# Optimization experiments

Hardware: AMD Instinct MI355X
Metric: run time of the kernel (lower is better)

The kernel has to match this reference:

```python
import jax, jax.numpy as jnp
import numpy as np

N = 100_000          # nodes
E = 3_200_000        # edges (avg degree 32)
EMB = 16             # item embedding dim
IN = EMB + 1         # concat(embed, scalar feature)
HID = 32             # GAT hidden size
NEMB = 1000          # embedding vocab
SLOPE = 0.2          # GATConv leaky_relu negative slope


def setup_inputs() -> dict:
    key = jax.random.key(0)
    ks = jax.random.split(key, 24)
    g = lambda k, shape, fan: jax.random.normal(k, shape, dtype=jnp.float32) * (1.0 / np.sqrt(fan))
    inp = {
        "x_ids": jax.random.randint(ks[0], (N,), 0, NEMB, dtype=jnp.int32),
        "x_feat": jax.random.normal(ks[1], (N, 1), dtype=jnp.float32),
        "src": jax.random.randint(ks[2], (E,), 0, N, dtype=jnp.int32),
        "dst": jax.random.randint(ks[3], (E,), 0, N, dtype=jnp.int32),
        "edge_attr": jax.random.normal(ks[4], (E, 1), dtype=jnp.float32),
        # embedding table
        "emb": g(ks[5], (NEMB, EMB), EMB),
        # GATConv 1 (in=17, out=32, heads=1, edge_dim=1)
        "W1": g(ks[6], (IN, HID), IN),
        "a_s1": g(ks[7], (HID,), HID),
        "a_d1": g(ks[8], (HID,), HID),
        "We1": g(ks[9], (1, HID), 1),
        "a_e1": g(ks[10], (HID,), HID),
        "b1": jnp.zeros((HID,), jnp.float32),
        # GATConv 2 (in=32, out=32)
        "W2": g(ks[11], (HID, HID), HID),
        "a_s2": g(ks[12], (HID,), HID),
        "a_d2": g(ks[13], (HID,), HID),
        "We2": g(ks[14], (1, HID), 1),
        "a_e2": g(ks[15], (HID,), HID),
        "b2": jnp.zeros((HID,), jnp.float32),
        # final linear (32 -> 1)
        "lin_w": g(ks[16], (HID, 1), HID),
        "lin_b": jnp.zeros((1,), jnp.float32),
    }
    return inp


def _gat_conv(x, src, dst, eattr, W, a_s, a_d, We, a_e, b):
    """PyG GATConv (heads=1, concat=True) with edge features, self-loops already added."""
    h = x @ W                                   # [N, HID]
    alpha_src = h @ a_s                         # [N]
    alpha_dst = h @ a_d                         # [N]
    alpha_edge = (eattr @ We) @ a_e             # [E']
    alpha = jax.nn.leaky_relu(alpha_src[src] + alpha_dst[dst] + alpha_edge, SLOPE)
    # segment softmax over incoming edges of each dst node
    m = jax.ops.segment_max(alpha, dst, num_segments=N)
    ex = jnp.exp(alpha - m[dst])
    denom = jax.ops.segment_sum(ex, dst, num_segments=N)
    coef = ex / (denom[dst] + 1e-16)
    out = jax.ops.segment_sum(coef[:, None] * h[src], dst, num_segments=N)
    return out + b


def reference(x_ids, x_feat, src, dst, edge_attr, emb,
              W1, a_s1, a_d1, We1, a_e1, b1,
              W2, a_s2, a_d2, We2, a_e2, b2,
              lin_w, lin_b):
    # embedding lookup + concat scalar feature -> [N, 17]
    x = jnp.concatenate([emb[x_ids], x_feat], axis=1)

    # add self-loops once; self-loop edge_attr = mean of incoming edge attrs (fill_value='mean')
    loop = jnp.arange(N, dtype=src.dtype)
    deg = jax.ops.segment_sum(jnp.ones((E,), x.dtype), dst, num_segments=N)
    loop_attr = jax.ops.segment_sum(edge_attr, dst, num_segments=N) / jnp.maximum(deg, 1.0)[:, None]
    src2 = jnp.concatenate([src, loop])
    dst2 = jnp.concatenate([dst, loop])
    ea2 = jnp.concatenate([edge_attr, loop_attr], axis=0)

    x = _gat_conv(x, src2, dst2, ea2, W1, a_s1, a_d1, We1, a_e1, b1)
    x = jax.nn.relu(x)  # dropout is identity in eval mode
    x = _gat_conv(x, src2, dst2, ea2, W2, a_s2, a_d2, We2, a_e2, b2)
    return x @ lin_w + lin_b  # [N, 1]
```

## Files before the change

kernel.cpp:

```cpp
#include <hip/hip_runtime.h>
#include <hip/hip_fp16.h>

#define NN 100000
#define EE 3200000
#define SLOPE 0.2f

#define BKN 128
constexpr int NBK = (NN + BKN - 1) / BKN;
#define CAP 4544
#define EPB 4096
constexpr int NBB = (EE + EPB - 1) / EPB;
constexpr int NBT = (NN + 255) / 256;
#define SUBN 1344
constexpr int NSB = NBK * 4;

__global__ void k_fat(const int* __restrict__ src, const int* __restrict__ dst,
                      const float* __restrict__ ea, int* __restrict__ cnt,
                      int2* __restrict__ stage,
                      const int* __restrict__ ids, const float* __restrict__ feat,
                      const float* __restrict__ emb, const float* __restrict__ W,
                      const float* __restrict__ avs, const float* __restrict__ avd,
                      __half* __restrict__ h, float* __restrict__ as_,
                      float* __restrict__ ad_) {
    __shared__ int hst[NBK];
    __shared__ int scl[NBK];
    __shared__ int gdel[NBK];
    __shared__ int aux[256];
    __shared__ int2 rec[EPB];
    __shared__ int addr[EPB];
    int t = threadIdx.x;
    if (blockIdx.x < NBB) {
        int base = blockIdx.x * EPB;
        int nedge = min(EPB, EE - base);
        for (int i = t; i < NBK; i += 256) hst[i] = 0;
        __syncthreads();
        int ds[16], ss[16]; float es[16];
#pragma unroll
        for (int j = 0; j < 16; j++) {
            int e = base + j * 256 + t;
            bool v = e < EE;
            ds[j] = v ? dst[e] : -1;
            ss[j] = v ? src[e] : 0;
            es[j] = v ? ea[e] : 0.f;
            if (v) atomicAdd(&hst[ds[j] >> 7], 1);
        }
        __syncthreads();
        int i0 = t * 4;
        int v0 = (i0 + 0 < NBK) ? hst[i0 + 0] : 0;
        int v1 = (i0 + 1 < NBK) ? hst[i0 + 1] : 0;
        int v2 = (i0 + 2 < NBK) ? hst[i0 + 2] : 0;
        int v3 = (i0 + 3 < NBK) ? hst[i0 + 3] : 0;
        int tsum = v0 + v1 + v2 + v3;
        aux[t] = tsum;
        __syncthreads();
        for (int off = 1; off < 256; off <<= 1) {
            int x = (t >= off) ? aux[t - off] : 0;
            __syncthreads();
            aux[t] += x;
            __syncthreads();
        }
        int ex = aux[t] - tsum;
        if (i0 + 0 < NBK) scl[i0 + 0] = ex;
        if (i0 + 1 < NBK) scl[i0 + 1] = ex + v0;
        if (i0 + 2 < NBK) scl[i0 + 2] = ex + v0 + v1;
        if (i0 + 3 < NBK) scl[i0 + 3] = ex + v0 + v1 + v2;
        __syncthreads();
        for (int i = t; i < NBK; i += 256) {
            int hh = hst[i];
            int g = hh ? atomicAdd(&cnt[i], hh) : 0;
            gdel[i] = (g + i * CAP) - scl[i];
        }
        __syncthreads();
#pragma unroll
        for (int j = 0; j < 16; j++) {
            if (ds[j] >= 0) {
                int bk = ds[j] >> 7;
                int pos = atomicAdd(&scl[bk], 1);
                int gpos = pos + gdel[bk];
                rec[pos] = make_int2(ss[j] | ((ds[j] & 127) << 17), __float_as_int(es[j]));
                addr[pos] = (gpos - bk * CAP < CAP) ? gpos : -1;
            }
        }
        __syncthreads();
        for (int i = t; i < nedge; i += 256) {
            int a = addr[i];
            if (a >= 0) stage[a] = rec[i];
        }
    } else {
        int n = (blockIdx.x - NBB) * 256 + t;
        if (n >= NN) return;
        float hv[32];
#pragma unroll
        for (int j = 0; j < 32; j++) hv[j] = 0.f;
        int id = ids[n];
        const float4* e4 = (const float4*)(emb + (size_t)id * 16);
#pragma unroll
        for (int k4 = 0; k4 < 4; k4++) {
            float4 xv = e4[k4];
            const float* wr = W + k4 * 4 * 32;
#pragma unroll
            for (int j = 0; j < 32; j++)
                hv[j] += xv.x * wr[j] + xv.y * wr[32 + j] + xv.z * wr[64 + j] + xv.w * wr[96 + j];
        }
        float f = feat[n];
#pragma unroll
        for (int j = 0; j < 32; j++) hv[j] += f * W[16 * 32 + j];
        float s = 0.f, d = 0.f;
#pragma unroll
        for (int j = 0; j < 32; j++) { s += hv[j] * avs[j]; d += hv[j] * avd[j]; }
        as_[n] = s;
        ad_[n] = d;
        __half2 tmp[16];
#pragma unroll
        for (int q = 0; q < 16; q++) tmp[q] = __floats2half2_rn(hv[2 * q], hv[2 * q + 1]);
        uint4* dst4 = (uint4*)(h + (size_t)n * 32);
        const uint4* s4 = (const uint4*)tmp;
#pragma unroll
        for (int q = 0; q < 4; q++) dst4[q] = s4[q];
    }
}

#define GATHER8(XB)                                                                   \
    for (int j = 0; j < m; j += 32) {                                                 \
        int2 p0 = XB[j + g];      int2 p1 = XB[j + 4 + g];                            \
        int2 p2 = XB[j + 8 + g];  int2 p3 = XB[j + 12 + g];                           \
        int2 p4 = XB[j + 16 + g]; int2 p5 = XB[j + 20 + g];                           \
        int2 p6 = XB[j + 24 + g]; int2 p7 = XB[j + 28 + g];                           \
        float2 h0 = __half22float2(*(const __half2*)(h + p0.x + cp));                 \
        float2 h1 = __half22float2(*(const __half2*)(h + p1.x + cp));                 \
        float2 h2 = __half22float2(*(const __half2*)(h + p2.x + cp));                 \
        float2 h3 = __half22float2(*(const __half2*)(h + p3.x + cp));                 \
        float2 h4 = __half22float2(*(const __half2*)(h + p4.x + cp));                 \
        float2 h5 = __half22float2(*(const __half2*)(h + p5.x + cp));                 \
        float2 h6 = __half22float2(*(const __half2*)(h + p6.x + cp));                 \
        float2 h7 = __half22float2(*(const __half2*)(h + p7.x + cp));                 \
        float w0 = __int_as_float(p0.y), w1 = __int_as_float(p1.y);                   \
        float w2 = __int_as_float(p2.y), w3 = __int_as_float(p3.y);                   \
        float w4 = __int_as_float(p4.y), w5 = __int_as_float(p5.y);                   \
        float w6 = __int_as_float(p6.y), w7 = __int_as_float(p7.y);                   \
        acc0.x += w0 * h0.x + w4 * h4.x; acc0.y += w0 * h0.y + w4 * h4.y;             \
        acc1.x += w1 * h1.x + w5 * h5.x; acc1.y += w1 * h1.y + w5 * h5.y;             \
        acc2.x += w2 * h2.x + w6 * h6.x; acc2.y += w2 * h2.y + w6 * h6.y;             \
        acc3.x += w3 * h3.x + w7 * h7.x; acc3.y += w3 * h3.y + w7 * h7.y;             \
    }

__global__ __launch_bounds__(256, 8) void k_l1(
    const int* __restrict__ cnt, const int2* __restrict__ stage,
    const __half* __restrict__ h, const float* __restrict__ as_,
    const float* __restrict__ ad_, const float* __restrict__ We,
    const float* __restrict__ ae, const float* __restrict__ bias,
    const float* __restrict__ W2, const float* __restrict__ avs2,
    const float* __restrict__ avd2, __half* __restrict__ hout,
    float* __restrict__ as2, float* __restrict__ ad2,
    int2* __restrict__ csr, int2* __restrict__ offs2) {
    __shared__ int2 ebuf[SUBN];
    __shared__ int2 xb[4][64];
    __shared__ float w2s[1024];
    __shared__ float xrow[4][32];
    __shared__ int ldeg[32];
    __shared__ float esum[32];
    __shared__ int starts[32];
    __shared__ int lcur[32];
    __shared__ int cnts[32];
    __shared__ float means[32];
    int t = threadIdx.x;
    int p = blockIdx.x;
    int b2 = (p & 7) * 391 + (p >> 3);
    int b = b2 >> 2, q = b2 & 3;
    int nbase = b * BKN + q * 32;
    int npb = min(32, NN - nbase);
    if (npb <= 0) return;
    int lane = t & 63;
    int wid = t >> 6;
    int g = lane >> 4;
    int cp = (lane & 15) * 2;
    int comp = lane & 31;
    float ce = We[comp] * ae[comp];
#pragma unroll
    for (int off = 1; off < 32; off <<= 1) ce += __shfl_xor(ce, off);

    if (t < 32) { ldeg[t] = 0; esum[t] = 0.f; }
    for (int i = t; i < 1024; i += 256) w2s[i] = W2[i];
    __syncthreads();
    int c = min(cnt[b], CAP);
    const int2* ep = stage + (size_t)b * CAP;
    for (int i = t; i < c; i += 256) {
        int2 e = ep[i];
        int dl = (e.x >> 17) & 127;
        if ((dl >> 5) == q) {
            atomicAdd(&ldeg[dl & 31], 1);
            atomicAdd(&esum[dl & 31], __int_as_float(e.y));
        }
    }
    __syncthreads();
    if (t < 64) {
        int l = lane;
        int dv = (l < npb) ? ldeg[l] + 1 : 0;
        int v = dv;
#pragma unroll
        for (int off = 1; off < 32; off <<= 1) {
            int x = __shfl_up(v, off);
            if (lane >= off) v += x;
        }
        if (l < 32) {
            int st = v - dv;
            starts[l] = st;
            lcur[l] = st;
            cnts[l] = dv;
            means[l] = esum[l] / fmaxf((float)ldeg[l], 1.0f);
        }
    }
    __syncthreads();
    for (int i = t; i < c; i += 256) {
        int2 e = ep[i];
        int dl = (e.x >> 17) & 127;
        if ((dl >> 5) == q) {
            int pos = atomicAdd(&lcur[dl & 31], 1);
            if (pos < SUBN) ebuf[pos] = make_int2(e.x & 0x1FFFF, e.y);
        }
    }
    __syncthreads();
    if (t < npb) {
        int pp = lcur[t];
        if (pp < SUBN) ebuf[pp] = make_int2(nbase + t, __float_as_int(means[t]));
    }
    __syncthreads();
    int tot = min(starts[31] + cnts[31], SUBN);
    int2* cw = csr + (size_t)b2 * SUBN;
    for (int i = t; i < tot; i += 256) cw[i] = ebuf[i];
    if (t < npb) {
        int st = starts[t];
        int cn = cnts[t];
        if (st >= SUBN) { st = 0; cn = 0; }
        else if (cn > SUBN - st) cn = SUBN - st;
        offs2[nbase + t] = make_int2(b2 * SUBN + st, cn);
    }

    for (int i2 = 0; i2 < 8; i2++) {
        int n = wid * 8 + i2;
        if (n >= npb) break;
        int gn = nbase + n;
        int base2 = starts[n];
        int cn = cnts[n];
        if (base2 >= SUBN) cn = 0;
        else if (cn > SUBN - base2) cn = SUBN - base2;
        float adn = ad_[gn];
        float2 acc0 = {0.f, 0.f}, acc1 = {0.f, 0.f}, acc2 = {0.f, 0.f}, acc3 = {0.f, 0.f};
        float exs = 0.f;
        for (int cb = 0; cb < cn; cb += 64) {
            int idx = cb + lane;
            bool val = idx < cn;
            int2 e = ebuf[base2 + (val ? idx : 0)];
            float a = as_[e.x] + adn + ce * __int_as_float(e.y);
            a = (a >= 0.f) ? a : SLOPE * a;
            float ex = val ? __expf(a) : 0.f;
            exs += ex;
            xb[wid][lane] = make_int2(e.x << 5, __float_as_int(ex));
            int m = min(cn - cb, 64);
            GATHER8(xb[wid])
        }
        float2 acc;
        acc.x = (acc0.x + acc1.x) + (acc2.x + acc3.x);
        acc.y = (acc0.y + acc1.y) + (acc2.y + acc3.y);
        acc.x += __shfl_xor(acc.x, 16); acc.y += __shfl_xor(acc.y, 16);
        acc.x += __shfl_xor(acc.x, 32); acc.y += __shfl_xor(acc.y, 32);
#pragma unroll
        for (int off = 1; off < 64; off <<= 1) exs += __shfl_xor(exs, off);
        float inv = 1.0f / (exs + 1e-16f);
        float ox = acc.x * inv + bias[cp];
        float oy = acc.y * inv + bias[cp + 1];
        ox = fmaxf(ox, 0.f);
        oy = fmaxf(oy, 0.f);
        if (lane < 16) { xrow[wid][cp] = ox; xrow[wid][cp + 1] = oy; }
        float hx = 0.f, hy = 0.f;
#pragma unroll
        for (int k = 0; k < 32; k++) {
            float xk = xrow[wid][k];
            hx += xk * w2s[k * 32 + cp];
            hy += xk * w2s[k * 32 + cp + 1];
        }
        float ps = hx * avs2[cp] + hy * avs2[cp + 1];
        float pd = hx * avd2[cp] + hy * avd2[cp + 1];
#pragma unroll
        for (int off = 1; off < 16; off <<= 1) {
            ps += __shfl_xor(ps, off);
            pd += __shfl_xor(pd, off);
        }
        if (lane == 0) { as2[gn] = ps; ad2[gn] = pd; }
        if (lane < 16)
            *(__half2*)(hout + ((size_t)gn << 5) + cp) = __floats2half2_rn(hx, hy);
    }
}

__global__ void k_gat(const int2* __restrict__ offs2, const int2* __restrict__ csr,
                      const __half* __restrict__ h, const float* __restrict__ as_,
                      const float* __restrict__ ad_,
                      const float* __restrict__ We, const float* __restrict__ ae,
                      const float* __restrict__ bias,
                      const float* __restrict__ lw, const float* __restrict__ lb,
                      float* __restrict__ out) {
    __shared__ int2 xb[4][64];
    int wid = threadIdx.x >> 6;
    int node = blockIdx.x * 4 + wid;
    int lane = threadIdx.x & 63;
    int comp = lane & 31;
    int cp = (lane & 15) * 2;
    int g = lane >> 4;
    float c = We[comp] * ae[comp];
#pragma unroll
    for (int off = 1; off < 32; off <<= 1) c += __shfl_xor(c, off);
    int2 oo = offs2[node];
    int base = oo.x;
    int cnt = oo.y;
    float adn = ad_[node];
    float2 acc0 = {0.f, 0.f}, acc1 = {0.f, 0.f}, acc2 = {0.f, 0.f}, acc3 = {0.f, 0.f};
    float exs = 0.f;
    for (int cb = 0; cb < cnt; cb += 64) {
        int idx = cb + lane;
        bool val = idx < cnt;
        int2 e = csr[base + (val ? idx : 0)];
        float a = as_[e.x] + adn + c * __int_as_float(e.y);
        a = (a >= 0.f) ? a : SLOPE * a;
        float ex = val ? __expf(a) : 0.f;
        exs += ex;
        xb[wid][lane] = make_int2(e.x << 5, __float_as_int(ex));
        int m = min(cnt - cb, 64);
        GATHER8(xb[wid])
    }
    float2 acc;
    acc.x = (acc0.x + acc1.x) + (acc2.x + acc3.x);
    acc.y = (acc0.y + acc1.y) + (acc2.y + acc3.y);
    acc.x += __shfl_xor(acc.x, 16); acc.y += __shfl_xor(acc.y, 16);
    acc.x += __shfl_xor(acc.x, 32); acc.y += __shfl_xor(acc.y, 32);
#pragma unroll
    for (int off = 1; off < 64; off <<= 1) exs += __shfl_xor(exs, off);
    float inv = 1.0f / (exs + 1e-16f);
    float ox = acc.x * inv + bias[cp];
    float oy = acc.y * inv + bias[cp + 1];
    float y = ox * lw[cp] + oy * lw[cp + 1];
#pragma unroll
    for (int off = 1; off < 16; off <<= 1) y += __shfl_xor(y, off);
    if (lane == 0) out[node] = y + lb[0];
}


extern "C" void kernel_launch(void* const* d_in, const int* in_sizes, int n_in,
                              void* d_out, int out_size, void* d_ws, size_t ws_size,
                              hipStream_t stream) {
    const int* x_ids = (const int*)d_in[0];
    const float* x_feat = (const float*)d_in[1];
    const int* src = (const int*)d_in[2];
    const int* dst = (const int*)d_in[3];
    const float* eattr = (const float*)d_in[4];
    const float* emb = (const float*)d_in[5];
    const float* W1 = (const float*)d_in[6];
    const float* a_s1 = (const float*)d_in[7];
    const float* a_d1 = (const float*)d_in[8];
    const float* We1 = (const float*)d_in[9];
    const float* a_e1 = (const float*)d_in[10];
    const float* b1 = (const float*)d_in[11];
    const float* W2 = (const float*)d_in[12];
    const float* a_s2 = (const float*)d_in[13];
    const float* a_d2 = (const float*)d_in[14];
    const float* We2 = (const float*)d_in[15];
    const float* a_e2 = (const float*)d_in[16];
    const float* b2 = (const float*)d_in[17];
    const float* lin_w = (const float*)d_in[18];
    const float* lin_b = (const float*)d_in[19];

    char* p = (char*)d_ws;
    auto alloc = [&](size_t bytes) {
        void* r = (void*)p;
        p += (bytes + 255) & ~(size_t)255;
        return r;
    };
    int* cnt = (int*)alloc(NBK * 4);
    int2* offs2 = (int2*)alloc((size_t)NN * 8);
    float* asb1 = (float*)alloc(NN * 4);
    float* adb1 = (float*)alloc(NN * 4);
    float* asb2 = (float*)alloc(NN * 4);
    float* adb2 = (float*)alloc(NN * 4);
    __half* h1 = (__half*)alloc((size_t)NN * 32 * 2);
    __half* h2 = (__half*)alloc((size_t)NN * 32 * 2);
    int2* csr = (int2*)alloc((size_t)NSB * SUBN * 8);
    int2* stage = (int2*)alloc((size_t)NBK * CAP * 8);
    (void)ws_size; (void)in_sizes; (void)n_in; (void)out_size;

    hipMemsetAsync(cnt, 0, NBK * 4, stream);

    k_fat<<<NBB + NBT, 256, 0, stream>>>(src, dst, eattr, cnt, stage,
                                         x_ids, x_feat, emb, W1, a_s1, a_d1,
                                         h1, asb1, adb1);
    k_l1<<<NSB, 256, 0, stream>>>(cnt, stage, h1, asb1, adb1,
                                  We1, a_e1, b1,
                                  W2, a_s2, a_d2, h2, asb2, adb2,
                                  csr, offs2);
    k_gat<<<(NN + 3) / 4, 256, 0, stream>>>(offs2, csr, h2, asb2, adb2,
                                            We2, a_e2, b2,
                                            lin_w, lin_b, (float*)d_out);
}
```

Baseline: 317.6 us.

## Bucket edges directly into 32-node global bins with atomics, drop block-local sort

Replaces the block-local histogram/scan/scatter partitioning with direct per-edge global atomicAdd into 3125 buckets of 32 destination nodes each, writing staged records straight to global memory. The layer-1 kernel now processes one 32-node bucket per block without filtering a 128-node bucket four times, loading edges into registers once. The gather macro is also narrowed from 8 to 4 edges per iteration. This trades coalesced staged writes and fewer atomics for many contended global atomics and scattered stores, and removes capacity clamps, so overflow safety now depends on CAPS/SUBN bounds and on the random degree distribution of the test inputs.

Measured after the change: 745.9 us. 2.35x slower.

```diff
diff --git a/kernel.cpp b/kernel.cpp
--- a/kernel.cpp
+++ b/kernel.cpp
@@ -5,14 +5,12 @@
 #define EE 3200000
 #define SLOPE 0.2f
 
-#define BKN 128
-constexpr int NBK = (NN + BKN - 1) / BKN;
-#define CAP 4544
-#define EPB 4096
-constexpr int NBB = (EE + EPB - 1) / EPB;
+#define CAPS 1344
+#define SUBN 1376
+constexpr int NSB2 = NN / 32;
+#define EPB2 2048
+constexpr int NAB = (EE + EPB2 - 1) / EPB2;
 constexpr int NBT = (NN + 255) / 256;
-#define SUBN 1344
-constexpr int NSB = NBK * 4;
 
 __global__ void k_fat(const int* __restrict__ src, const int* __restrict__ dst,
                       const float* __restrict__ ea, int* __restrict__ cnt,
@@ -22,72 +20,23 @@
                       const float* __restrict__ avs, const float* __restrict__ avd,
                       __half* __restrict__ h, float* __restrict__ as_,
                       float* __restrict__ ad_) {
-    __shared__ int hst[NBK];
-    __shared__ int scl[NBK];
-    __shared__ int gdel[NBK];
-    __shared__ int aux[256];
-    __shared__ int2 rec[EPB];
-    __shared__ int addr[EPB];
     int t = threadIdx.x;
-    if (blockIdx.x < NBB) {
-        int base = blockIdx.x * EPB;
-        int nedge = min(EPB, EE - base);
-        for (int i = t; i < NBK; i += 256) hst[i] = 0;
-        __syncthreads();
-        int ds[16], ss[16]; float es[16];
-#pragma unroll
-        for (int j = 0; j < 16; j++) {
+    if (blockIdx.x < NAB) {
+        int base = blockIdx.x * EPB2;
+#pragma unroll
+        for (int j = 0; j < 8; j++) {
             int e = base + j * 256 + t;
-            bool v = e < EE;
-            ds[j] = v ? dst[e] : -1;
-            ss[j] = v ? src[e] : 0;
-            es[j] = v ? ea[e] : 0.f;
-            if (v) atomicAdd(&hst[ds[j] >> 7], 1);
-        }
-        __syncthreads();
-        int i0 = t * 4;
-        int v0 = (i0 + 0 < NBK) ? hst[i0 + 0] : 0;
-        int v1 = (i0 + 1 < NBK) ? hst[i0 + 1] : 0;
-        int v2 = (i0 + 2 < NBK) ? hst[i0 + 2] : 0;
-        int v3 = (i0 + 3 < NBK) ? hst[i0 + 3] : 0;
-        int tsum = v0 + v1 + v2 + v3;
-        aux[t] = tsum;
-        __syncthreads();
-        for (int off = 1; off < 256; off <<= 1) {
-            int x = (t >= off) ? aux[t - off] : 0;
-            __syncthreads();
-            aux[t] += x;
-            __syncthreads();
-        }
-        int ex = aux[t] - tsum;
-        if (i0 + 0 < NBK) scl[i0 + 0] = ex;
-        if (i0 + 1 < NBK) scl[i0 + 1] = ex + v0;
-        if (i0 + 2 < NBK) scl[i0 + 2] = ex + v0 + v1;
-        if (i0 + 3 < NBK) scl[i0 + 3] = ex + v0 + v1 + v2;
-        __syncthreads();
-        for (int i = t; i < NBK; i += 256) {
-            int hh = hst[i];
-            int g = hh ? atomicAdd(&cnt[i], hh) : 0;
-            gdel[i] = (g + i * CAP) - scl[i];
-        }
-        __syncthreads();
-#pragma unroll
-        for (int j = 0; j < 16; j++) {
-            if (ds[j] >= 0) {
-                int bk = ds[j] >> 7;
-                int pos = atomicAdd(&scl[bk], 1);
-                int gpos = pos + gdel[bk];
-                rec[pos] = make_int2(ss[j] | ((ds[j] & 127) << 17), __float_as_int(es[j]));
-                addr[pos] = (gpos - bk * CAP < CAP) ? gpos : -1;
+            if (e < EE) {
+                int d = dst[e];
+                int bk = d >> 5;
+                int pos = atomicAdd(&cnt[bk], 1);
+                if (pos < CAPS)
+                    stage[(size_t)bk * CAPS + pos] =
+                        make_int2(src[e] | ((d & 31) << 17), __float_as_int(ea[e]));
             }
         }
-        __syncthreads();
-        for (int i = t; i < nedge; i += 256) {
-            int a = addr[i];
-            if (a >= 0) stage[a] = rec[i];
-        }
     } else {
-        int n = (blockIdx.x - NBB) * 256 + t;
+        int n = (blockIdx.x - NAB) * 256 + t;
         if (n >= NN) return;
         float hv[32];
 #pragma unroll
@@ -120,28 +69,22 @@
     }
 }
 
-#define GATHER8(XB)                                                                   \
-    for (int j = 0; j < m; j += 32) {                                                 \
-        int2 p0 = XB[j + g];      int2 p1 = XB[j + 4 + g];                            \
-        int2 p2 = XB[j + 8 + g];  int2 p3 = XB[j + 12 + g];                           \
-        int2 p4 = XB[j + 16 + g]; int2 p5 = XB[j + 20 + g];                           \
-        int2 p6 = XB[j + 24 + g]; int2 p7 = XB[j + 28 + g];                           \
+#define GATHER4(XB)                                                                   \
+    for (int j = 0; j < m; j += 16) {                                                 \
+        int2 p0 = XB[j + g];                                                          \
+        int2 p1 = XB[j + 4 + g];                                                      \
+        int2 p2 = XB[j + 8 + g];                                                      \
+        int2 p3 = XB[j + 12 + g];                                                     \
         float2 h0 = __half22float2(*(const __half2*)(h + p0.x + cp));                 \
         float2 h1 = __half22float2(*(const __half2*)(h + p1.x + cp));                 \
         float2 h2 = __half22float2(*(const __half2*)(h + p2.x + cp));                 \
         float2 h3 = __half22float2(*(const __half2*)(h + p3.x + cp));                 \
-        float2 h4 = __half22float2(*(const __half2*)(h + p4.x + cp));                 \
-        float2 h5 = __half22float2(*(const __half2*)(h + p5.x + cp));                 \
-        float2 h6 = __half22float2(*(const __half2*)(h + p6.x + cp));                 \
-        float2 h7 = __half22float2(*(const __half2*)(h + p7.x + cp));                 \
         float w0 = __int_as_float(p0.y), w1 = __int_as_float(p1.y);                   \
         float w2 = __int_as_float(p2.y), w3 = __int_as_float(p3.y);                   \
-        float w4 = __int_as_float(p4.y), w5 = __int_as_float(p5.y);                   \
-        float w6 = __int_as_float(p6.y), w7 = __int_as_float(p7.y);                   \
-        acc0.x += w0 * h0.x + w4 * h4.x; acc0.y += w0 * h0.y + w4 * h4.y;             \
-        acc1.x += w1 * h1.x + w5 * h5.x; acc1.y += w1 * h1.y + w5 * h5.y;             \
-        acc2.x += w2 * h2.x + w6 * h6.x; acc2.y += w2 * h2.y + w6 * h6.y;             \
-        acc3.x += w3 * h3.x + w7 * h7.x; acc3.y += w3 * h3.y + w7 * h7.y;             \
+        acc0.x += w0 * h0.x; acc0.y += w0 * h0.y;                                     \
+        acc1.x += w1 * h1.x; acc1.y += w1 * h1.y;                                     \
+        acc2.x += w2 * h2.x; acc2.y += w2 * h2.y;                                     \
+        acc3.x += w3 * h3.x; acc3.y += w3 * h3.y;                                     \
     }
 
 __global__ __launch_bounds__(256, 8) void k_l1(
@@ -164,12 +107,8 @@
     __shared__ int cnts[32];
     __shared__ float means[32];
     int t = threadIdx.x;
-    int p = blockIdx.x;
-    int b2 = (p & 7) * 391 + (p >> 3);
-    int b = b2 >> 2, q = b2 & 3;
-    int nbase = b * BKN + q * 32;
-    int npb = min(32, NN - nbase);
-    if (npb <= 0) return;
+    int bb = blockIdx.x;
+    int nbase = bb * 32;
     int lane = t & 63;
     int wid = t >> 6;
     int g = lane >> 4;
@@ -182,20 +121,26 @@
     if (t < 32) { ldeg[t] = 0; esum[t] = 0.f; }
     for (int i = t; i < 1024; i += 256) w2s[i] = W2[i];
     __syncthreads();
-    int c = min(cnt[b], CAP);
-    const int2* ep = stage + (size_t)b * CAP;
-    for (int i = t; i < c; i += 256) {
-        int2 e = ep[i];
-        int dl = (e.x >> 17) & 127;
-        if ((dl >> 5) == q) {
-            atomicAdd(&ldeg[dl & 31], 1);
-            atomicAdd(&esum[dl & 31], __int_as_float(e.y));
+    int c = min(cnt[bb], CAPS);
+    const int2* ep = stage + (size_t)bb * CAPS;
+    int2 er[6];
+#pragma unroll
+    for (int j = 0; j < 6; j++) {
+        int i = j * 256 + t;
+        er[j] = (i < c) ? ep[i] : make_int2(-1, 0);
+    }
+#pragma unroll
+    for (int j = 0; j < 6; j++) {
+        if (er[j].x >= 0) {
+            int dl = (er[j].x >> 17) & 31;
+            atomicAdd(&ldeg[dl], 1);
+            atomicAdd(&esum[dl], __int_as_float(er[j].y));
         }
     }
     __syncthreads();
     if (t < 64) {
         int l = lane;
-        int dv = (l < npb) ? ldeg[l] + 1 : 0;
+        int dv = (l < 32) ? ldeg[l] + 1 : 0;
         int v = dv;
 #pragma unroll
         for (int off = 1; off < 32; off <<= 1) {
@@ -211,39 +156,29 @@
         }
     }
     __syncthreads();
-    for (int i = t; i < c; i += 256) {
-        int2 e = ep[i];
-        int dl = (e.x >> 17) & 127;
-        if ((dl >> 5) == q) {
-            int pos = atomicAdd(&lcur[dl & 31], 1);
-            if (pos < SUBN) ebuf[pos] = make_int2(e.x & 0x1FFFF, e.y);
-        }
-    }
-    __syncthreads();
-    if (t < npb) {
-        int pp = lcur[t];
-        if (pp < SUBN) ebuf[pp] = make_int2(nbase + t, __float_as_int(means[t]));
-    }
-    __syncthreads();
-    int tot = min(starts[31] + cnts[31], SUBN);
-    int2* cw = csr + (size_t)b2 * SUBN;
+#pragma unroll
+    for (int j = 0; j < 6; j++) {
+        if (er[j].x >= 0) {
+            int dl = (er[j].x >> 17) & 31;
+            int pos = atomicAdd(&lcur[dl], 1);
+            ebuf[pos] = make_int2(er[j].x & 0x1FFFF, er[j].y);
+        }
+    }
+    __syncthreads();
+    if (t < 32)
+        ebuf[lcur[t]] = make_int2(nbase + t, __float_as_int(means[t]));
+    __syncthreads();
+    int tot = starts[31] + cnts[31];
+    int2* cw = csr + (size_t)bb * SUBN;
     for (int i = t; i < tot; i += 256) cw[i] = ebuf[i];
-    if (t < npb) {
-        int st = starts[t];
-        int cn = cnts[t];
-        if (st >= SUBN) { st = 0; cn = 0; }
-        else if (cn > SUBN - st) cn = SUBN - st;
-        offs2[nbase + t] = make_int2(b2 * SUBN + st, cn);
-    }
+    if (t < 32)
+        offs2[nbase + t] = make_int2(bb * SUBN + starts[t], cnts[t]);
 
     for (int i2 = 0; i2 < 8; i2++) {
         int n = wid * 8 + i2;
-        if (n >= npb) break;
         int gn = nbase + n;
         int base2 = starts[n];
         int cn = cnts[n];
-        if (base2 >= SUBN) cn = 0;
-        else if (cn > SUBN - base2) cn = SUBN - base2;
         float adn = ad_[gn];
         float2 acc0 = {0.f, 0.f}, acc1 = {0.f, 0.f}, acc2 = {0.f, 0.f}, acc3 = {0.f, 0.f};
         float exs = 0.f;
@@ -257,7 +192,7 @@
             exs += ex;
             xb[wid][lane] = make_int2(e.x << 5, __float_as_int(ex));
             int m = min(cn - cb, 64);
-            GATHER8(xb[wid])
+            GATHER4(xb[wid])
         }
         float2 acc;
         acc.x = (acc0.x + acc1.x) + (acc2.x + acc3.x);
@@ -325,7 +260,7 @@
         exs += ex;
         xb[wid][lane] = make_int2(e.x << 5, __float_as_int(ex));
         int m = min(cnt - cb, 64);
-        GATHER8(xb[wid])
+        GATHER4(xb[wid])
     }
     float2 acc;
     acc.x = (acc0.x + acc1.x) + (acc2.x + acc3.x);
@@ -374,7 +309,7 @@
         p += (bytes + 255) & ~(size_t)255;
         return r;
     };
-    int* cnt = (int*)alloc(NBK * 4);
+    int* cnt = (int*)alloc(NSB2 * 4);
     int2* offs2 = (int2*)alloc((size_t)NN * 8);
     float* asb1 = (float*)alloc(NN * 4);
     float* adb1 = (float*)alloc(NN * 4);
@@ -382,19 +317,19 @@
     float* adb2 = (float*)alloc(NN * 4);
     __half* h1 = (__half*)alloc((size_t)NN * 32 * 2);
     __half* h2 = (__half*)alloc((size_t)NN * 32 * 2);
-    int2* csr = (int2*)alloc((size_t)NSB * SUBN * 8);
-    int2* stage = (int2*)alloc((size_t)NBK * CAP * 8);
+    int2* csr = (int2*)alloc((size_t)NSB2 * SUBN * 8);
+    int2* stage = (int2*)alloc((size_t)NSB2 * CAPS * 8);
     (void)ws_size; (void)in_sizes; (void)n_in; (void)out_size;
 
-    hipMemsetAsync(cnt, 0, NBK * 4, stream);
-
-    k_fat<<<NBB + NBT, 256, 0, stream>>>(src, dst, eattr, cnt, stage,
+    hipMemsetAsync(cnt, 0, NSB2 * 4, stream);
+
+    k_fat<<<NAB + NBT, 256, 0, stream>>>(src, dst, eattr, cnt, stage,
                                          x_ids, x_feat, emb, W1, a_s1, a_d1,
                                          h1, asb1, adb1);
-    k_l1<<<NSB, 256, 0, stream>>>(cnt, stage, h1, asb1, adb1,
-                                  We1, a_e1, b1,
-                                  W2, a_s2, a_d2, h2, asb2, adb2,
-                                  csr, offs2);
+    k_l1<<<NSB2, 256, 0, stream>>>(cnt, stage, h1, asb1, adb1,
+                                   We1, a_e1, b1,
+                                   W2, a_s2, a_d2, h2, asb2, adb2,
+                                   csr, offs2);
     k_gat<<<(NN + 3) / 4, 256, 0, stream>>>(offs2, csr, h2, asb2, adb2,
                                             We2, a_e2, b2,
                                             lin_w, lin_b, (float*)d_out);
```

## Scatter edges directly to stage, use wave-shuffle scan, shrink gather unroll

Applied to the files above, without the earlier changes.

The binning kernel no longer stages per-block records and addresses in LDS. Each thread now writes its packed edge straight to the global stage buffer, which cuts about 48KB of shared memory per block and one sync pass, but the global writes are no longer coalesced. The block prefix scan now uses wave shuffles plus a 4-entry cross-wave sum instead of a barrier-heavy LDS scan. The gather macro is reduced from 8 to 4 loads per iteration, which avoids wasted work when a chunk holds fewer than 32 edges, at the cost of less memory-level parallelism.

Result: no change. 316.7 us (-0.3%).

```diff
diff --git a/kernel.cpp b/kernel.cpp
--- a/kernel.cpp
+++ b/kernel.cpp
@@ -25,13 +25,11 @@
     __shared__ int hst[NBK];
     __shared__ int scl[NBK];
     __shared__ int gdel[NBK];
-    __shared__ int aux[256];
-    __shared__ int2 rec[EPB];
-    __shared__ int addr[EPB];
+    __shared__ int wsum[4];
     int t = threadIdx.x;
     if (blockIdx.x < NBB) {
         int base = blockIdx.x * EPB;
-        int nedge = min(EPB, EE - base);
+        int lane = t & 63, wid = t >> 6;
         for (int i = t; i < NBK; i += 256) hst[i] = 0;
         __syncthreads();
         int ds[16], ss[16]; float es[16];
@@ -51,15 +49,18 @@
         int v2 = (i0 + 2 < NBK) ? hst[i0 + 2] : 0;
         int v3 = (i0 + 3 < NBK) ? hst[i0 + 3] : 0;
         int tsum = v0 + v1 + v2 + v3;
-        aux[t] = tsum;
-        __syncthreads();
-        for (int off = 1; off < 256; off <<= 1) {
-            int x = (t >= off) ? aux[t - off] : 0;
-            __syncthreads();
-            aux[t] += x;
-            __syncthreads();
-        }
-        int ex = aux[t] - tsum;
+        int incl = tsum;
+#pragma unroll
+        for (int off = 1; off < 64; off <<= 1) {
+            int x = __shfl_up(incl, off);
+            if (lane >= off) incl += x;
+        }
+        if (lane == 63) wsum[wid] = incl;
+        __syncthreads();
+        int wpre = 0;
+#pragma unroll
+        for (int w = 0; w < 4; w++) wpre += (w < wid) ? wsum[w] : 0;
+        int ex = wpre + incl - tsum;
         if (i0 + 0 < NBK) scl[i0 + 0] = ex;
         if (i0 + 1 < NBK) scl[i0 + 1] = ex + v0;
         if (i0 + 2 < NBK) scl[i0 + 2] = ex + v0 + v1;
@@ -77,14 +78,10 @@
                 int bk = ds[j] >> 7;
                 int pos = atomicAdd(&scl[bk], 1);
                 int gpos = pos + gdel[bk];
-                rec[pos] = make_int2(ss[j] | ((ds[j] & 127) << 17), __float_as_int(es[j]));
-                addr[pos] = (gpos - bk * CAP < CAP) ? gpos : -1;
+                if (gpos - bk * CAP < CAP)
+                    stage[gpos] = make_int2(ss[j] | ((ds[j] & 127) << 17),
+                                            __float_as_int(es[j]));
             }
-        }
-        __syncthreads();
-        for (int i = t; i < nedge; i += 256) {
-            int a = addr[i];
-            if (a >= 0) stage[a] = rec[i];
         }
     } else {
         int n = (blockIdx.x - NBB) * 256 + t;
@@ -120,28 +117,22 @@
     }
 }
 
-#define GATHER8(XB)                                                                   \
-    for (int j = 0; j < m; j += 32) {                                                 \
-        int2 p0 = XB[j + g];      int2 p1 = XB[j + 4 + g];                            \
-        int2 p2 = XB[j + 8 + g];  int2 p3 = XB[j + 12 + g];                           \
-        int2 p4 = XB[j + 16 + g]; int2 p5 = XB[j + 20 + g];                           \
-        int2 p6 = XB[j + 24 + g]; int2 p7 = XB[j + 28 + g];                           \
+#define GATHER4(XB)                                                                   \
+    for (int j = 0; j < m; j += 16) {                                                 \
+        int2 p0 = XB[j + g];                                                          \
+        int2 p1 = XB[j + 4 + g];                                                      \
+        int2 p2 = XB[j + 8 + g];                                                      \
+        int2 p3 = XB[j + 12 + g];                                                     \
         float2 h0 = __half22float2(*(const __half2*)(h + p0.x + cp));                 \
         float2 h1 = __half22float2(*(const __half2*)(h + p1.x + cp));                 \
         float2 h2 = __half22float2(*(const __half2*)(h + p2.x + cp));                 \
         float2 h3 = __half22float2(*(const __half2*)(h + p3.x + cp));                 \
-        float2 h4 = __half22float2(*(const __half2*)(h + p4.x + cp));                 \
-        float2 h5 = __half22float2(*(const __half2*)(h + p5.x + cp));                 \
-        float2 h6 = __half22float2(*(const __half2*)(h + p6.x + cp));                 \
-        float2 h7 = __half22float2(*(const __half2*)(h + p7.x + cp));                 \
         float w0 = __int_as_float(p0.y), w1 = __int_as_float(p1.y);                   \
         float w2 = __int_as_float(p2.y), w3 = __int_as_float(p3.y);                   \
-        float w4 = __int_as_float(p4.y), w5 = __int_as_float(p5.y);                   \
-        float w6 = __int_as_float(p6.y), w7 = __int_as_float(p7.y);                   \
-        acc0.x += w0 * h0.x + w4 * h4.x; acc0.y += w0 * h0.y + w4 * h4.y;             \
-        acc1.x += w1 * h1.x + w5 * h5.x; acc1.y += w1 * h1.y + w5 * h5.y;             \
-        acc2.x += w2 * h2.x + w6 * h6.x; acc2.y += w2 * h2.y + w6 * h6.y;             \
-        acc3.x += w3 * h3.x + w7 * h7.x; acc3.y += w3 * h3.y + w7 * h7.y;             \
+        acc0.x += w0 * h0.x; acc0.y += w0 * h0.y;                                     \
+        acc1.x += w1 * h1.x; acc1.y += w1 * h1.y;                                     \
+        acc2.x += w2 * h2.x; acc2.y += w2 * h2.y;                                     \
+        acc3.x += w3 * h3.x; acc3.y += w3 * h3.y;                                     \
     }
 
 __global__ __launch_bounds__(256, 8) void k_l1(
@@ -257,7 +248,7 @@
             exs += ex;
             xb[wid][lane] = make_int2(e.x << 5, __float_as_int(ex));
             int m = min(cn - cb, 64);
-            GATHER8(xb[wid])
+            GATHER4(xb[wid])
         }
         float2 acc;
         acc.x = (acc0.x + acc1.x) + (acc2.x + acc3.x);
@@ -325,7 +316,7 @@
         exs += ex;
         xb[wid][lane] = make_int2(e.x << 5, __float_as_int(ex));
         int m = min(cnt - cb, 64);
-        GATHER8(xb[wid])
+        GATHER4(xb[wid])
     }
     float2 acc;
     acc.x = (acc0.x + acc1.x) + (acc2.x + acc3.x);
```
